# Kernel optimization log

Measured on AMD Instinct MI355X. Metric: run time of the kernel, lower is better.

Reference implementation:

```python
import jax, jax.numpy as jnp
import numpy as np

DEPTH, HEADS, DIM_HEAD = 3, 8, 64
DIM = 512
MAX_SEQ = 2048
INNER = HEADS * DIM_HEAD  # 512
FF_HID = 4 * DIM          # 2048
EPS = 1e-5


def sparsemax(z):
    # z: (..., n); sparsemax projection onto the simplex (Martins & Astudillo 2016)
    n = z.shape[-1]
    z_sorted = jnp.flip(jnp.sort(z, axis=-1), axis=-1)            # descending
    cs = jnp.cumsum(z_sorted, axis=-1)
    ks = jnp.arange(1, n + 1, dtype=z.dtype)
    support = 1.0 + ks * z_sorted > cs                            # bool
    k_z = jnp.sum(support, axis=-1, keepdims=True)                # int support size
    cs_k = jnp.take_along_axis(cs, k_z - 1, axis=-1)
    tau = (cs_k - 1.0) / k_z.astype(z.dtype)
    return jnp.maximum(z - tau, 0.0)


def layernorm(x, g, b):
    mu = jnp.mean(x, axis=-1, keepdims=True)
    var = jnp.mean(jnp.square(x - mu), axis=-1, keepdims=True)
    return (x - mu) * jax.lax.rsqrt(var + EPS) * g + b


def setup_inputs() -> dict:
    key = jax.random.key(0)
    ks = jax.random.split(key, 12)
    s = 0.02
    inp = {
        "x": jax.random.normal(ks[0], (8, 1024, DIM), dtype=jnp.float32),
        "proj_w": jax.random.normal(ks[1], (DIM, DIM), dtype=jnp.float32) * s,
        "proj_b": jnp.zeros((DIM,), dtype=jnp.float32),
        "pos_emb": jax.random.normal(ks[2], (MAX_SEQ, DIM), dtype=jnp.float32) * s,
        "ln1_g": jnp.ones((DEPTH, DIM), dtype=jnp.float32),
        "ln1_b": jnp.zeros((DEPTH, DIM), dtype=jnp.float32),
        "wqkv": jax.random.normal(ks[3], (DEPTH, DIM, 3 * INNER), dtype=jnp.float32) * s,
        "wout": jax.random.normal(ks[4], (DEPTH, INNER, DIM), dtype=jnp.float32) * s,
        "bout": jnp.zeros((DEPTH, DIM), dtype=jnp.float32),
        "ln2_g": jnp.ones((DEPTH, DIM), dtype=jnp.float32),
        "ln2_b": jnp.zeros((DEPTH, DIM), dtype=jnp.float32),
        "w1": jax.random.normal(ks[5], (DEPTH, DIM, 2 * FF_HID), dtype=jnp.float32) * s,
        "b1": jnp.zeros((DEPTH, 2 * FF_HID), dtype=jnp.float32),
        "w2": jax.random.normal(ks[6], (DEPTH, FF_HID, DIM), dtype=jnp.float32) * s,
        "b2": jnp.zeros((DEPTH, DIM), dtype=jnp.float32),
    }
    return inp


def reference(x, proj_w, proj_b, pos_emb, ln1_g, ln1_b, wqkv, wout, bout,
              ln2_g, ln2_b, w1, b1, w2, b2):
    B, S, D = x.shape
    scale = DIM_HEAD ** -0.5
    x = x @ proj_w + proj_b                       # projection
    x = x + pos_emb[:S][None, :, :]               # positional embedding
    for l in range(DEPTH):
        # --- attention block (Residual(PreNorm(Attention))) ---
        h = layernorm(x, ln1_g[l], ln1_b[l])
        qkv = h @ wqkv[l]                         # (B,S,3*INNER)
        q, k, v = jnp.split(qkv, 3, axis=-1)
        rs = lambda t: t.reshape(B, S, HEADS, DIM_HEAD).transpose(0, 2, 1, 3)
        q, k, v = rs(q), rs(k), rs(v)             # (B,H,S,Dh)
        sim = jnp.einsum('bhid,bhjd->bhij', q, k) * scale
        attn = sparsemax(sim)
        out = jnp.einsum('bhij,bhjd->bhid', attn, v)
        out = out.transpose(0, 2, 1, 3).reshape(B, S, INNER)
        x = x + (out @ wout[l] + bout[l])
        # --- feedforward block (Residual(PreNorm(GEGLU FFN))) ---
        h = layernorm(x, ln2_g[l], ln2_b[l])
        hh = h @ w1[l] + b1[l]                    # (B,S,2*FF_HID)
        a, g = jnp.split(hh, 2, axis=-1)
        ff = (a * jax.nn.gelu(g, approximate=False)) @ w2[l] + b2[l]
        x = x + ff
    return jnp.mean(x, axis=1)                    # (B, D) mean pool
```

## Files before the change

kernel.cpp:

```cpp
#include <hip/hip_runtime.h>
#include <stdint.h>

typedef unsigned short u16;
typedef __attribute__((ext_vector_type(8))) short short8;
typedef __attribute__((ext_vector_type(4))) float f32x4;

__device__ __forceinline__ float bf2f(u16 u){
  union { unsigned u; float f; } v; v.u = ((unsigned)u) << 16; return v.f;
}
__device__ __forceinline__ u16 f2bf(float f){
  union { float f; unsigned u; } v; v.f = f;
  unsigned u = v.u;
  return (u16)((u + 0x7FFFu + ((u >> 16) & 1u)) >> 16);
}
__device__ __forceinline__ void g2lds16(const u16* g, u16* lds){
  __builtin_amdgcn_global_load_lds(
      (const __attribute__((address_space(1))) unsigned int*)g,
      (__attribute__((address_space(3))) unsigned int*)lds, 16, 0, 0);
}
__device__ __forceinline__ float gelu_fast(float g){
  float u2 = g * (1.5957691216057308f + 0.0713548162726f * g * g);
  return g * __builtin_amdgcn_rcpf(1.0f + __expf(-u2));
}

__global__ void k_flag(const unsigned* __restrict__ ln1g, int* __restrict__ flag){
  if (threadIdx.x == 0 && blockIdx.x == 0)
    *flag = (ln1g[0] == 0x3F800000u) ? 0 : 1;
}

__global__ void k_cvt_f32(const void* __restrict__ src, float* __restrict__ dst, int n,
                          const int* __restrict__ flag){
  int i = blockIdx.x * blockDim.x + threadIdx.x;
  if (i < n) dst[i] = (*flag) ? bf2f(((const u16*)src)[i]) : ((const float*)src)[i];
}
__global__ void k_cvt_f32_v8(const void* __restrict__ src, float* __restrict__ dst,
                             const int* __restrict__ flag){
  int i = blockIdx.x * blockDim.x + threadIdx.x;
  if (*flag){
    short8 v = ((const short8*)src)[i];
    float o[8];
    #pragma unroll
    for (int j = 0; j < 8; ++j) o[j] = bf2f((u16)v[j]);
    ((float4*)dst)[i*2]   = *(const float4*)o;
    ((float4*)dst)[i*2+1] = *(const float4*)(o + 4);
  } else {
    ((float4*)dst)[i*2]   = ((const float4*)src)[i*2];
    ((float4*)dst)[i*2+1] = ((const float4*)src)[i*2+1];
  }
}
__global__ void k_cvt_bf16(const void* __restrict__ src, u16* __restrict__ dst, int n,
                           const int* __restrict__ flag){
  int i = blockIdx.x * blockDim.x + threadIdx.x;
  if (i < n) dst[i] = (*flag) ? ((const u16*)src)[i] : f2bf(((const float*)src)[i]);
}
__global__ void k_cvt_bf16_v8(const void* __restrict__ src, u16* __restrict__ dst,
                              const int* __restrict__ flag){
  int i = blockIdx.x * blockDim.x + threadIdx.x;
  if (*flag){
    ((uint4*)dst)[i] = ((const uint4*)src)[i];
  } else {
    float4 a = ((const float4*)src)[i*2];
    float4 b = ((const float4*)src)[i*2+1];
    u16 o[8] = { f2bf(a.x), f2bf(a.y), f2bf(a.z), f2bf(a.w),
                 f2bf(b.x), f2bf(b.y), f2bf(b.z), f2bf(b.w) };
    ((uint4*)dst)[i] = *(const uint4*)o;
  }
}

__global__ void k_transpose(const void* __restrict__ src, u16* __restrict__ dst,
                            int K, int N, const int* __restrict__ flag){
  __shared__ u16 tile[32][33];
  int n0 = blockIdx.x * 32, k0 = blockIdx.y * 32;
  size_t zsrc = (size_t)blockIdx.z * K * N;
  size_t zdst = (size_t)blockIdx.z * N * K;
  int tx = threadIdx.x & 31, ty = threadIdx.x >> 5;
  bool isbf = (*flag) != 0;
  const float* sf = (const float*)src; const u16* sb = (const u16*)src;
  #pragma unroll
  for (int p = 0; p < 4; ++p){
    int kk = k0 + p*8 + ty, nn = n0 + tx;
    size_t idx = zsrc + (size_t)kk * N + nn;
    tile[tx][p*8+ty] = isbf ? sb[idx] : f2bf(sf[idx]);
  }
  __syncthreads();
  #pragma unroll
  for (int p = 0; p < 4; ++p){
    int nn = n0 + p*8 + ty, kk = k0 + tx;
    dst[zdst + (size_t)nn * K + kk] = tile[p*8+ty][tx];
  }
}

__global__ __launch_bounds__(256) void k_ln(const float* __restrict__ x,
                                            const float* __restrict__ g,
                                            const float* __restrict__ b,
                                            u16* __restrict__ out){
  int wv = threadIdx.x >> 6, lane = threadIdx.x & 63;
  int row = blockIdx.x * 4 + wv;
  const float* xr = x + (size_t)row * 512 + lane * 8;
  float4 v0 = *(const float4*)xr;
  float4 v1 = *(const float4*)(xr + 4);
  float s  = v0.x+v0.y+v0.z+v0.w + v1.x+v1.y+v1.z+v1.w;
  float ss = v0.x*v0.x+v0.y*v0.y+v0.z*v0.z+v0.w*v0.w
           + v1.x*v1.x+v1.y*v1.y+v1.z*v1.z+v1.w*v1.w;
  #pragma unroll
  for (int off = 1; off < 64; off <<= 1){ s += __shfl_xor(s, off, 64); ss += __shfl_xor(ss, off, 64); }
  float mu = s * (1.f/512.f);
  float var = ss * (1.f/512.f) - mu*mu;
  float rs = rsqrtf(var + 1e-5f);
  const float* gp = g + lane*8; const float* bp = b + lane*8;
  float4 g0 = *(const float4*)gp, g1 = *(const float4*)(gp+4);
  float4 b0 = *(const float4*)bp, b1 = *(const float4*)(bp+4);
  u16 o[8];
  o[0]=f2bf((v0.x-mu)*rs*g0.x+b0.x); o[1]=f2bf((v0.y-mu)*rs*g0.y+b0.y);
  o[2]=f2bf((v0.z-mu)*rs*g0.z+b0.z); o[3]=f2bf((v0.w-mu)*rs*g0.w+b0.w);
  o[4]=f2bf((v1.x-mu)*rs*g1.x+b1.x); o[5]=f2bf((v1.y-mu)*rs*g1.y+b1.y);
  o[6]=f2bf((v1.z-mu)*rs*g1.z+b1.z); o[7]=f2bf((v1.w-mu)*rs*g1.w+b1.w);
  *(uint4*)(out + (size_t)row*512 + lane*8) = *(const uint4*)o;
}

__global__ __launch_bounds__(256) void k_gemm(const u16* __restrict__ A,
                                              const u16* __restrict__ Wt, int K, int mode,
                                              float* __restrict__ xres, u16* __restrict__ out16,
                                              const float* __restrict__ bias,
                                              const float* __restrict__ pos){
  __shared__ u16 As[128*64];
  __shared__ u16 Bs[128*64];
  const int tid = threadIdx.x;
  const int wv = tid >> 6, lane = tid & 63;
  const int lm = lane & 15, lq = lane >> 4;
  const int wm = (wv >> 1) * 64, wn = (wv & 1) * 64;
  const int m0 = blockIdx.y * 128, n0 = blockIdx.x * 128;
  const int lrow = lane >> 3;
  const int scol = ((lane & 7) ^ lrow) << 3;
  f32x4 acc[4][4];
  #pragma unroll
  for (int i = 0; i < 4; ++i)
    #pragma unroll
    for (int j = 0; j < 4; ++j){ f32x4 z = {0.f,0.f,0.f,0.f}; acc[i][j] = z; }

  for (int k0 = 0; k0 < K; k0 += 64){
    #pragma unroll
    for (int it = 0; it < 4; ++it){
      int ci = wv*4 + it;
      int row = ci*8 + lrow;
      g2lds16(&A [(size_t)(m0 + row) * K + k0 + scol], &As[ci*512]);
      g2lds16(&Wt[(size_t)(n0 + row) * K + k0 + scol], &Bs[ci*512]);
    }
    __syncthreads();
    #pragma unroll
    for (int kk = 0; kk < 2; ++kk){
      short8 af[4], bf[4];
      #pragma unroll
      for (int t = 0; t < 4; ++t){
        int cs = ((kk*4 + lq) ^ (lm & 7)) << 3;
        af[t] = *(const short8*)&As[(wm + t*16 + lm)*64 + cs];
        bf[t] = *(const short8*)&Bs[(wn + t*16 + lm)*64 + cs];
      }
      #pragma unroll
      for (int i = 0; i < 4; ++i)
        #pragma unroll
        for (int j = 0; j < 4; ++j)
          acc[i][j] = __builtin_amdgcn_mfma_f32_16x16x32_bf16(af[i], bf[j], acc[i][j], 0, 0, 0);
    }
    __syncthreads();
  }
  #pragma unroll
  for (int i = 0; i < 4; ++i)
    #pragma unroll
    for (int j = 0; j < 4; ++j)
      #pragma unroll
      for (int r = 0; r < 4; ++r){
        int row = m0 + wm + i*16 + lq*4 + r;
        int col = n0 + wn + j*16 + lm;
        float v = acc[i][j][r];
        if (mode == 0){
          xres[(size_t)row*512 + col] = v + bias[col] + pos[(size_t)(row & 1023)*512 + col];
        } else if (mode == 1){
          int part = col >> 9, within = col & 511;
          int head = within >> 6, dh = within & 63;
          int b = row >> 10, s = row & 1023;
          int bh = b*8 + head;
          size_t o;
          if (part < 2) o = (size_t)part*4194304 + (((size_t)bh*1024 + s) << 6) + dh;
          else          o = (size_t)8388608 + (size_t)bh*65536 + (size_t)dh*1024 + s;
          out16[o] = f2bf(v);
        } else {
          size_t idx = (size_t)row*512 + col;
          xres[idx] = xres[idx] + v + bias[col];
        }
      }
}

__global__ __launch_bounds__(256) void k_gemm64(const u16* __restrict__ A,
                                                const u16* __restrict__ Wt, int K, int mode,
                                                float* __restrict__ xres,
                                                const float* __restrict__ bias,
                                                const float* __restrict__ pos){
  __shared__ u16 As[64*64];
  __shared__ u16 Bs[128*64];
  const int tid = threadIdx.x;
  const int wv = tid >> 6, lane = tid & 63;
  const int lm = lane & 15, lq = lane >> 4;
  const int wm = (wv >> 1) * 32, wn = (wv & 1) * 64;
  const int m0 = blockIdx.y * 64, n0 = blockIdx.x * 128;
  const int lrow = lane >> 3;
  const int scol = ((lane & 7) ^ lrow) << 3;
  f32x4 acc[2][4];
  #pragma unroll
  for (int i = 0; i < 2; ++i)
    #pragma unroll
    for (int j = 0; j < 4; ++j){ f32x4 z = {0.f,0.f,0.f,0.f}; acc[i][j] = z; }

  for (int k0 = 0; k0 < K; k0 += 64){
    #pragma unroll
    for (int it = 0; it < 2; ++it){
      int ci = wv*2 + it;
      int row = ci*8 + lrow;
      g2lds16(&A[(size_t)(m0 + row) * K + k0 + scol], &As[ci*512]);
    }
    #pragma unroll
    for (int it = 0; it < 4; ++it){
      int ci = wv*4 + it;
      int row = ci*8 + lrow;
      g2lds16(&Wt[(size_t)(n0 + row) * K + k0 + scol], &Bs[ci*512]);
    }
    __syncthreads();
    #pragma unroll
    for (int kk = 0; kk < 2; ++kk){
      short8 af[2], bf[4];
      int cs = ((kk*4 + lq) ^ (lm & 7)) << 3;
      #pragma unroll
      for (int t = 0; t < 2; ++t)
        af[t] = *(const short8*)&As[(wm + t*16 + lm)*64 + cs];
      #pragma unroll
      for (int t = 0; t < 4; ++t)
        bf[t] = *(const short8*)&Bs[(wn + t*16 + lm)*64 + cs];
      #pragma unroll
      for (int i = 0; i < 2; ++i)
        #pragma unroll
        for (int j = 0; j < 4; ++j)
          acc[i][j] = __builtin_amdgcn_mfma_f32_16x16x32_bf16(af[i], bf[j], acc[i][j], 0, 0, 0);
    }
    __syncthreads();
  }
  #pragma unroll
  for (int i = 0; i < 2; ++i)
    #pragma unroll
    for (int j = 0; j < 4; ++j)
      #pragma unroll
      for (int r = 0; r < 4; ++r){
        int row = m0 + wm + i*16 + lq*4 + r;
        int col = n0 + wn + j*16 + lm;
        float v = acc[i][j][r];
        if (mode == 0){
          xres[(size_t)row*512 + col] = v + bias[col] + pos[(size_t)(row & 1023)*512 + col];
        } else {
          size_t idx = (size_t)row*512 + col;
          xres[idx] = xres[idx] + v + bias[col];
        }
      }
}

__global__ __launch_bounds__(256) void k_ff1_geglu64(const u16* __restrict__ A,
                                                     const u16* __restrict__ W1t,
                                                     const float* __restrict__ b1,
                                                     u16* __restrict__ ffh){
  __shared__ u16 As[64*64];
  __shared__ u16 Ba[128*64];
  __shared__ u16 Bg[128*64];
  const int tid = threadIdx.x;
  const int wv = tid >> 6, lane = tid & 63;
  const int lm = lane & 15, lq = lane >> 4;
  const int wm = (wv >> 1) * 32, wn = (wv & 1) * 64;
  const int m0 = blockIdx.y * 64, n0 = blockIdx.x * 128;
  const int lrow = lane >> 3;
  const int scol = ((lane & 7) ^ lrow) << 3;
  const int K = 512;
  f32x4 aa[2][4], ag[2][4];
  #pragma unroll
  for (int i = 0; i < 2; ++i)
    #pragma unroll
    for (int j = 0; j < 4; ++j){ f32x4 z = {0.f,0.f,0.f,0.f}; aa[i][j] = z; ag[i][j] = z; }
  for (int k0 = 0; k0 < K; k0 += 64){
    #pragma unroll
    for (int it = 0; it < 2; ++it){
      int ci = wv*2 + it;
      int row = ci*8 + lrow;
      g2lds16(&A[(size_t)(m0 + row) * K + k0 + scol], &As[ci*512]);
    }
    #pragma unroll
    for (int it = 0; it < 4; ++it){
      int ci = wv*4 + it;
      int row = ci*8 + lrow;
      g2lds16(&W1t[(size_t)(n0 + row) * K + k0 + scol],        &Ba[ci*512]);
      g2lds16(&W1t[(size_t)(2048 + n0 + row) * K + k0 + scol], &Bg[ci*512]);
    }
    __syncthreads();
    #pragma unroll
    for (int kk = 0; kk < 2; ++kk){
      short8 af[2], ba[4], bg[4];
      int cs = ((kk*4 + lq) ^ (lm & 7)) << 3;
      #pragma unroll
      for (int t = 0; t < 2; ++t)
        af[t] = *(const short8*)&As[(wm + t*16 + lm)*64 + cs];
      #pragma unroll
      for (int t = 0; t < 4; ++t){
        ba[t] = *(const short8*)&Ba[(wn + t*16 + lm)*64 + cs];
        bg[t] = *(const short8*)&Bg[(wn + t*16 + lm)*64 + cs];
      }
      #pragma unroll
      for (int i = 0; i < 2; ++i)
        #pragma unroll
        for (int j = 0; j < 4; ++j){
          aa[i][j] = __builtin_amdgcn_mfma_f32_16x16x32_bf16(af[i], ba[j], aa[i][j], 0, 0, 0);
          ag[i][j] = __builtin_amdgcn_mfma_f32_16x16x32_bf16(af[i], bg[j], ag[i][j], 0, 0, 0);
        }
    }
    __syncthreads();
  }
  #pragma unroll
  for (int i = 0; i < 2; ++i)
    #pragma unroll
    for (int j = 0; j < 4; ++j)
      #pragma unroll
      for (int r = 0; r < 4; ++r){
        int row = m0 + wm + i*16 + lq*4 + r;
        int n = n0 + wn + j*16 + lm;
        float a = aa[i][j][r] + b1[n];
        float g = ag[i][j][r] + b1[2048 + n];
        ffh[(size_t)row*2048 + n] = f2bf(a * gelu_fast(g));
      }
}

__global__ __launch_bounds__(256) void k_attn2(const u16* __restrict__ qb,
                                               const u16* __restrict__ kb,
                                               const u16* __restrict__ vt,
                                               u16* __restrict__ aout){
  __shared__ u16 Sm[16*1024];
  const int tid = threadIdx.x;
  const int wv = tid >> 6, lane = tid & 63;
  const int lm = lane & 15, lq = lane >> 4;
  int fid = blockIdx.x;
  int nf = (fid & 7) * 512 + (fid >> 3);
  const int bh = nf >> 6;
  const int q0 = (nf & 63) * 16;
  const size_t base = (size_t)bh * 65536;
  const u16* qp = &qb[base + (size_t)(q0 + lm)*64 + lq*8];
  short8 qf0 = *(const short8*)qp;
  short8 qf1 = *(const short8*)(qp + 32);
  for (int kt = 0; kt < 16; ++kt){
    const u16* kp = &kb[base + (size_t)(kt*64 + wv*16 + lm)*64 + lq*8];
    short8 kf0 = *(const short8*)kp;
    short8 kf1 = *(const short8*)(kp + 32);
    f32x4 a = {0.f,0.f,0.f,0.f};
    a = __builtin_amdgcn_mfma_f32_16x16x32_bf16(qf0, kf0, a, 0, 0, 0);
    a = __builtin_amdgcn_mfma_f32_16x16x32_bf16(qf1, kf1, a, 0, 0, 0);
    int col = kt*64 + wv*16 + lm;
    int cc = col >> 3, c7 = col & 7;
    #pragma unroll
    for (int r = 0; r < 4; ++r){
      int row = lq*4 + r;
      Sm[row*1024 + ((cc ^ (row & 7)) << 3) + c7] = f2bf(a[r] * 0.125f);
    }
  }
  __syncthreads();
  #pragma unroll 1
  for (int rr = 0; rr < 4; ++rr){
    int row = wv*4 + rr;
    int r7 = row & 7;
    u16* lo = &Sm[row*1024 + ((lane ^ r7) << 3)];
    u16* hi = &Sm[row*1024 + (((64 + lane) ^ r7) << 3)];
    u16 zb[16];
    *(uint4*)zb       = *(const uint4*)lo;
    *(uint4*)(zb + 8) = *(const uint4*)hi;
    float z[16];
    #pragma unroll
    for (int i = 0; i < 16; ++i) z[i] = bf2f(zb[i]);
    float s0 = 0.f;
    #pragma unroll
    for (int i = 0; i < 16; ++i) s0 += z[i];
    #pragma unroll
    for (int off = 1; off < 64; off <<= 1) s0 += __shfl_xor(s0, off, 64);
    float tau = (s0 - 1.0f) * (1.0f/1024.0f);
    int prevc = 1024;
    #pragma unroll 1
    for (int it = 0; it < 32; ++it){
      float sz = 0.f; int c = 0;
      #pragma unroll
      for (int i = 0; i < 16; ++i){
        bool aq = z[i] > tau;
        sz += aq ? z[i] : 0.f;
        c  += (int)__popcll(__ballot(aq));
      }
      if (c >= prevc) break;
      #pragma unroll
      for (int off = 1; off < 64; off <<= 1) sz += __shfl_xor(sz, off, 64);
      tau = (sz - 1.0f) / (float)c;
      prevc = c;
    }
    u16 pb[16];
    #pragma unroll
    for (int i = 0; i < 16; ++i){
      float p = z[i] - tau;
      pb[i] = f2bf(p > 0.f ? p : 0.f);
    }
    *(uint4*)lo = *(const uint4*)pb;
    *(uint4*)hi = *(const uint4*)(pb + 8);
  }
  __syncthreads();
  f32x4 acc = {0.f,0.f,0.f,0.f};
  const u16* vrow = &vt[base + (size_t)(wv*16 + lm)*1024 + lq*8];
  for (int k0 = 0; k0 < 1024; k0 += 32){
    int cc = (k0 >> 3) + lq;
    short8 pa = *(const short8*)&Sm[lm*1024 + ((cc ^ (lm & 7)) << 3)];
    short8 vb = *(const short8*)(vrow + k0);
    acc = __builtin_amdgcn_mfma_f32_16x16x32_bf16(pa, vb, acc, 0, 0, 0);
  }
  int b = bh >> 3, h = bh & 7;
  #pragma unroll
  for (int r = 0; r < 4; ++r){
    int s = q0 + lq*4 + r;
    aout[((size_t)(b*1024 + s))*512 + h*64 + wv*16 + lm] = f2bf(acc[r]);
  }
}

__global__ __launch_bounds__(256) void k_pool1(const float* __restrict__ xres,
                                               float* __restrict__ part){
  int b = blockIdx.y, ch = blockIdx.x, tid = threadIdx.x;
  float a0 = 0.f, a1 = 0.f;
  for (int i = 0; i < 64; ++i){
    const float* r = xres + ((size_t)(b*1024 + ch*64 + i)) * 512;
    a0 += r[tid]; a1 += r[tid + 256];
  }
  part[((size_t)(b*16 + ch))*512 + tid]       = a0;
  part[((size_t)(b*16 + ch))*512 + tid + 256] = a1;
}
__global__ __launch_bounds__(512) void k_pool2(const float* __restrict__ part,
                                               void* __restrict__ out,
                                               const int* __restrict__ flag){
  int b = blockIdx.x, d = threadIdx.x;
  float s = 0.f;
  for (int c = 0; c < 16; ++c) s += part[((size_t)(b*16 + c))*512 + d];
  s *= (1.0f/1024.0f);
  if (*flag) ((u16*)out)[b*512 + d] = f2bf(s);
  else       ((float*)out)[b*512 + d] = s;
}

extern "C" void kernel_launch(void* const* d_in, const int* in_sizes, int n_in,
                              void* d_out, int out_size, void* d_ws, size_t ws_size,
                              hipStream_t stream){
  (void)in_sizes; (void)n_in; (void)out_size; (void)ws_size;
  char* w = (char*)d_ws;
  size_t off = 0;
  auto alloc = [&](size_t bytes) -> char* {
    char* p = w + off;
    off += (bytes + 255) & ~(size_t)255;
    return p;
  };
  int*   flag  = (int*)  alloc(4);
  float* xres  = (float*)alloc((size_t)8192*512*4);
  u16*   hb    = (u16*)  alloc((size_t)8192*512*2);
  u16*   qb    = (u16*)  alloc((size_t)8388608);
  u16*   kb    = (u16*)  alloc((size_t)8388608);
  u16*   vtb   = (u16*)  alloc((size_t)8388608);
  u16*   aoutb = (u16*)  alloc((size_t)8388608);
  u16*   ffh   = qb;
  u16*   pwT   = (u16*)  alloc((size_t)512*512*2);
  u16*   wqkvT = (u16*)  alloc((size_t)3*1536*512*2);
  u16*   woutT = (u16*)  alloc((size_t)3*512*512*2);
  u16*   w1T   = (u16*)  alloc((size_t)3*4096*512*2);
  u16*   w2T   = (u16*)  alloc((size_t)3*512*2048*2);
  float* posf  = (float*)alloc((size_t)1024*512*4);
  float* pbf   = (float*)alloc(512*4);
  float* ln1gf = (float*)alloc(1536*4);
  float* ln1bf = (float*)alloc(1536*4);
  float* ln2gf = (float*)alloc(1536*4);
  float* ln2bf = (float*)alloc(1536*4);
  float* boutf = (float*)alloc(1536*4);
  float* b1f   = (float*)alloc(12288*4);
  float* b2f   = (float*)alloc(1536*4);
  float* part  = (float*)alloc((size_t)8*16*512*4);

  const void* x_raw = d_in[0];  const void* projw = d_in[1];  const void* projb = d_in[2];
  const void* pose  = d_in[3];  const void* ln1g  = d_in[4];  const void* ln1b  = d_in[5];
  const void* wqkv  = d_in[6];  const void* wout  = d_in[7];  const void* bout  = d_in[8];
  const void* ln2g  = d_in[9];  const void* ln2b  = d_in[10]; const void* w1    = d_in[11];
  const void* b1    = d_in[12]; const void* w2    = d_in[13]; const void* b2    = d_in[14];

  k_flag<<<1, 1, 0, stream>>>((const unsigned*)ln1g, flag);

  k_transpose<<<dim3(16, 16, 1), 256, 0, stream>>>(projw, pwT,   512,  512, flag);
  k_transpose<<<dim3(48, 16, 3), 256, 0, stream>>>(wqkv,  wqkvT, 512, 1536, flag);
  k_transpose<<<dim3(16, 16, 3), 256, 0, stream>>>(wout,  woutT, 512,  512, flag);
  k_transpose<<<dim3(128,16, 3), 256, 0, stream>>>(w1,    w1T,   512, 4096, flag);
  k_transpose<<<dim3(16, 64, 3), 256, 0, stream>>>(w2,    w2T,  2048,  512, flag);

  k_cvt_f32<<<2,    256, 0, stream>>>(projb, pbf,    512,    flag);
  k_cvt_f32_v8<<<256, 256, 0, stream>>>(pose, posf, flag);
  k_cvt_f32<<<6,    256, 0, stream>>>(ln1g,  ln1gf,  1536,   flag);
  k_cvt_f32<<<6,    256, 0, stream>>>(ln1b,  ln1bf,  1536,   flag);
  k_cvt_f32<<<6,    256, 0, stream>>>(ln2g,  ln2gf,  1536,   flag);
  k_cvt_f32<<<6,    256, 0, stream>>>(ln2b,  ln2bf,  1536,   flag);
  k_cvt_f32<<<6,    256, 0, stream>>>(bout,  boutf,  1536,   flag);
  k_cvt_f32<<<48,   256, 0, stream>>>(b1,    b1f,    12288,  flag);
  k_cvt_f32<<<6,    256, 0, stream>>>(b2,    b2f,    1536,   flag);
  k_cvt_bf16_v8<<<2048, 256, 0, stream>>>(x_raw, hb, flag);

  k_gemm64<<<dim3(4, 128), 256, 0, stream>>>(hb, pwT, 512, 0, xres, pbf, posf);

  for (int l = 0; l < 3; ++l){
    k_ln<<<2048, 256, 0, stream>>>(xres, ln1gf + l*512, ln1bf + l*512, hb);
    k_gemm<<<dim3(12, 64), 256, 0, stream>>>(hb, wqkvT + (size_t)l*1536*512, 512, 1,
                                             nullptr, qb, nullptr, nullptr);
    k_attn2<<<dim3(4096), 256, 0, stream>>>(qb, kb, vtb, aoutb);
    k_gemm64<<<dim3(4, 128), 256, 0, stream>>>(aoutb, woutT + (size_t)l*512*512, 512, 2,
                                               xres, boutf + l*512, nullptr);
    k_ln<<<2048, 256, 0, stream>>>(xres, ln2gf + l*512, ln2bf + l*512, hb);
    k_ff1_geglu64<<<dim3(16, 128), 256, 0, stream>>>(hb, w1T + (size_t)l*4096*512,
                                                     b1f + l*4096, ffh);
    k_gemm64<<<dim3(4, 128), 256, 0, stream>>>(ffh, w2T + (size_t)l*512*2048, 2048, 2,
                                               xres, b2f + l*512, nullptr);
  }
  k_pool1<<<dim3(16, 8), 256, 0, stream>>>(xres, part);
  k_pool2<<<8, 512, 0, stream>>>(part, d_out, flag);
}
```

Before: 1.065 ms.

## Widen attention block to 16 waves with split-K PV and LDS reduction

The sparsemax attention kernel now launches with 1024 threads instead of 256. Each of the 16 waves computes one 64-column key tile of QK^T, handles one row of the sparsemax threshold iteration, and computes a quarter of the PV product per output slice. The four partial PV results are reduced through a new shared-memory buffer before the bf16 store. The idea is to cut each wave's serial loops and raise parallelism per block, at the cost of more LDS, an extra barrier, and possibly lower occupancy. The sparsemax loop also now reduces and uses a fast reciprocal before its convergence check.

```diff
diff --git a/kernel.cpp b/kernel.cpp
--- a/kernel.cpp
+++ b/kernel.cpp
@@ -332,11 +332,12 @@
       }
 }
 
-__global__ __launch_bounds__(256) void k_attn2(const u16* __restrict__ qb,
-                                               const u16* __restrict__ kb,
-                                               const u16* __restrict__ vt,
-                                               u16* __restrict__ aout){
+__global__ __launch_bounds__(1024) void k_attn2(const u16* __restrict__ qb,
+                                                const u16* __restrict__ kb,
+                                                const u16* __restrict__ vt,
+                                                u16* __restrict__ aout){
   __shared__ u16 Sm[16*1024];
+  __shared__ float Pp[4*16*64];
   const int tid = threadIdx.x;
   const int wv = tid >> 6, lane = tid & 63;
   const int lm = lane & 15, lq = lane >> 4;
@@ -348,26 +349,28 @@
   const u16* qp = &qb[base + (size_t)(q0 + lm)*64 + lq*8];
   short8 qf0 = *(const short8*)qp;
   short8 qf1 = *(const short8*)(qp + 32);
-  for (int kt = 0; kt < 16; ++kt){
-    const u16* kp = &kb[base + (size_t)(kt*64 + wv*16 + lm)*64 + lq*8];
-    short8 kf0 = *(const short8*)kp;
-    short8 kf1 = *(const short8*)(kp + 32);
-    f32x4 a = {0.f,0.f,0.f,0.f};
-    a = __builtin_amdgcn_mfma_f32_16x16x32_bf16(qf0, kf0, a, 0, 0, 0);
-    a = __builtin_amdgcn_mfma_f32_16x16x32_bf16(qf1, kf1, a, 0, 0, 0);
-    int col = kt*64 + wv*16 + lm;
-    int cc = col >> 3, c7 = col & 7;
-    #pragma unroll
-    for (int r = 0; r < 4; ++r){
-      int row = lq*4 + r;
-      Sm[row*1024 + ((cc ^ (row & 7)) << 3) + c7] = f2bf(a[r] * 0.125f);
+  {
+    const int kt = wv;
+    #pragma unroll
+    for (int j = 0; j < 4; ++j){
+      const u16* kp = &kb[base + (size_t)(kt*64 + j*16 + lm)*64 + lq*8];
+      short8 kf0 = *(const short8*)kp;
+      short8 kf1 = *(const short8*)(kp + 32);
+      f32x4 a = {0.f,0.f,0.f,0.f};
+      a = __builtin_amdgcn_mfma_f32_16x16x32_bf16(qf0, kf0, a, 0, 0, 0);
+      a = __builtin_amdgcn_mfma_f32_16x16x32_bf16(qf1, kf1, a, 0, 0, 0);
+      int col = kt*64 + j*16 + lm;
+      int cc = col >> 3, c7 = col & 7;
+      #pragma unroll
+      for (int r = 0; r < 4; ++r){
+        int row = lq*4 + r;
+        Sm[row*1024 + ((cc ^ (row & 7)) << 3) + c7] = f2bf(a[r] * 0.125f);
+      }
     }
   }
   __syncthreads();
-  #pragma unroll 1
-  for (int rr = 0; rr < 4; ++rr){
-    int row = wv*4 + rr;
-    int r7 = row & 7;
+  {
+    const int row = wv, r7 = row & 7;
     u16* lo = &Sm[row*1024 + ((lane ^ r7) << 3)];
     u16* hi = &Sm[row*1024 + (((64 + lane) ^ r7) << 3)];
     u16 zb[16];
@@ -392,10 +395,10 @@
         sz += aq ? z[i] : 0.f;
         c  += (int)__popcll(__ballot(aq));
       }
+      #pragma unroll
+      for (int off = 1; off < 64; off <<= 1) sz += __shfl_xor(sz, off, 64);
+      tau = (sz - 1.0f) * __builtin_amdgcn_rcpf((float)c);
       if (c >= prevc) break;
-      #pragma unroll
-      for (int off = 1; off < 64; off <<= 1) sz += __shfl_xor(sz, off, 64);
-      tau = (sz - 1.0f) / (float)c;
       prevc = c;
     }
     u16 pb[16];
@@ -405,22 +408,31 @@
       pb[i] = f2bf(p > 0.f ? p : 0.f);
     }
     *(uint4*)lo = *(const uint4*)pb;
-    *(uint4*)hi = *(const uint4*)(pb + 8);
+    *(uint4*)(hi) = *(const uint4*)(pb + 8);
   }
   __syncthreads();
-  f32x4 acc = {0.f,0.f,0.f,0.f};
-  const u16* vrow = &vt[base + (size_t)(wv*16 + lm)*1024 + lq*8];
-  for (int k0 = 0; k0 < 1024; k0 += 32){
-    int cc = (k0 >> 3) + lq;
-    short8 pa = *(const short8*)&Sm[lm*1024 + ((cc ^ (lm & 7)) << 3)];
-    short8 vb = *(const short8*)(vrow + k0);
-    acc = __builtin_amdgcn_mfma_f32_16x16x32_bf16(pa, vb, acc, 0, 0, 0);
-  }
-  int b = bh >> 3, h = bh & 7;
-  #pragma unroll
-  for (int r = 0; r < 4; ++r){
-    int s = q0 + lq*4 + r;
-    aout[((size_t)(b*1024 + s))*512 + h*64 + wv*16 + lm] = f2bf(acc[r]);
+  {
+    const int ds = wv & 3, kc = wv >> 2;
+    f32x4 acc = {0.f,0.f,0.f,0.f};
+    const u16* vrow = &vt[base + (size_t)(ds*16 + lm)*1024 + lq*8];
+    #pragma unroll
+    for (int k0 = kc*256; k0 < kc*256 + 256; k0 += 32){
+      int cc = (k0 >> 3) + lq;
+      short8 pa = *(const short8*)&Sm[lm*1024 + ((cc ^ (lm & 7)) << 3)];
+      short8 vb = *(const short8*)(vrow + k0);
+      acc = __builtin_amdgcn_mfma_f32_16x16x32_bf16(pa, vb, acc, 0, 0, 0);
+    }
+    #pragma unroll
+    for (int r = 0; r < 4; ++r)
+      Pp[(kc*16 + lq*4 + r)*64 + ds*16 + lm] = acc[r];
+  }
+  __syncthreads();
+  {
+    int s = tid >> 6, d = tid & 63;
+    int o = s*64 + d;
+    float v = Pp[o] + Pp[1024 + o] + Pp[2048 + o] + Pp[3072 + o];
+    int b = bh >> 3, h = bh & 7;
+    aout[((size_t)(b*1024 + q0 + s))*512 + h*64 + d] = f2bf(v);
   }
 }
 
@@ -512,7 +524,7 @@
     k_ln<<<2048, 256, 0, stream>>>(xres, ln1gf + l*512, ln1bf + l*512, hb);
     k_gemm<<<dim3(12, 64), 256, 0, stream>>>(hb, wqkvT + (size_t)l*1536*512, 512, 1,
                                              nullptr, qb, nullptr, nullptr);
-    k_attn2<<<dim3(4096), 256, 0, stream>>>(qb, kb, vtb, aoutb);
+    k_attn2<<<dim3(4096), 1024, 0, stream>>>(qb, kb, vtb, aoutb);
     k_gemm64<<<dim3(4, 128), 256, 0, stream>>>(aoutb, woutT + (size_t)l*512*512, 512, 2,
                                                xres, boutf + l*512, nullptr);
     k_ln<<<2048, 256, 0, stream>>>(xres, ln2gf + l*512, ln2bf + l*512, hb);
```

Measured after the change: 1.100 ms. 1.03x slower.

## Warm-start sparsemax threshold from row statistics and process two rows at once

Applied to the files above, without the earlier changes.

The sparsemax threshold search now starts from an estimate built from the row's mean, standard deviation and max (a Gaussian-tail heuristic) instead of tau=(sum-1)/n. It then iterates a Newton-style update from above or below, capped at 48 iterations. Two rows are processed together per wave so the shuffle reductions and ballots interleave and expose more instruction-level parallelism. The aim is fewer sequential threshold iterations per row. The cost is extra register pressure, and the heuristic start may take more iterations on some inputs or converge to a slightly different tau. An unused conversion kernel is also deleted.

```diff
diff --git a/kernel.cpp b/kernel.cpp
--- a/kernel.cpp
+++ b/kernel.cpp
@@ -47,11 +47,6 @@
     ((float4*)dst)[i*2]   = ((const float4*)src)[i*2];
     ((float4*)dst)[i*2+1] = ((const float4*)src)[i*2+1];
   }
-}
-__global__ void k_cvt_bf16(const void* __restrict__ src, u16* __restrict__ dst, int n,
-                           const int* __restrict__ flag){
-  int i = blockIdx.x * blockDim.x + threadIdx.x;
-  if (i < n) dst[i] = (*flag) ? ((const u16*)src)[i] : f2bf(((const float*)src)[i]);
 }
 __global__ void k_cvt_bf16_v8(const void* __restrict__ src, u16* __restrict__ dst,
                               const int* __restrict__ flag){
@@ -365,47 +360,89 @@
   }
   __syncthreads();
   #pragma unroll 1
-  for (int rr = 0; rr < 4; ++rr){
-    int row = wv*4 + rr;
-    int r7 = row & 7;
-    u16* lo = &Sm[row*1024 + ((lane ^ r7) << 3)];
-    u16* hi = &Sm[row*1024 + (((64 + lane) ^ r7) << 3)];
-    u16 zb[16];
-    *(uint4*)zb       = *(const uint4*)lo;
-    *(uint4*)(zb + 8) = *(const uint4*)hi;
-    float z[16];
-    #pragma unroll
-    for (int i = 0; i < 16; ++i) z[i] = bf2f(zb[i]);
-    float s0 = 0.f;
-    #pragma unroll
-    for (int i = 0; i < 16; ++i) s0 += z[i];
-    #pragma unroll
-    for (int off = 1; off < 64; off <<= 1) s0 += __shfl_xor(s0, off, 64);
-    float tau = (s0 - 1.0f) * (1.0f/1024.0f);
-    int prevc = 1024;
+  for (int pp = 0; pp < 2; ++pp){
+    int rowA = wv*4 + pp*2, rowB = rowA + 1;
+    int aA7 = rowA & 7, aB7 = rowB & 7;
+    u16* loA = &Sm[rowA*1024 + ((lane ^ aA7) << 3)];
+    u16* hiA = &Sm[rowA*1024 + (((64 + lane) ^ aA7) << 3)];
+    u16* loB = &Sm[rowB*1024 + ((lane ^ aB7) << 3)];
+    u16* hiB = &Sm[rowB*1024 + (((64 + lane) ^ aB7) << 3)];
+    u16 zbA[16], zbB[16];
+    *(uint4*)zbA       = *(const uint4*)loA;
+    *(uint4*)(zbA + 8) = *(const uint4*)hiA;
+    *(uint4*)zbB       = *(const uint4*)loB;
+    *(uint4*)(zbB + 8) = *(const uint4*)hiB;
+    float zA[16], zB[16];
+    #pragma unroll
+    for (int i = 0; i < 16; ++i){ zA[i] = bf2f(zbA[i]); zB[i] = bf2f(zbB[i]); }
+    float sA = 0.f, ssA = 0.f, mxA = zA[0];
+    float sB = 0.f, ssB = 0.f, mxB = zB[0];
+    #pragma unroll
+    for (int i = 0; i < 16; ++i){
+      sA += zA[i]; ssA = fmaf(zA[i], zA[i], ssA); mxA = fmaxf(mxA, zA[i]);
+      sB += zB[i]; ssB = fmaf(zB[i], zB[i], ssB); mxB = fmaxf(mxB, zB[i]);
+    }
+    #pragma unroll
+    for (int off = 1; off < 64; off <<= 1){
+      sA  += __shfl_xor(sA,  off, 64);  sB  += __shfl_xor(sB,  off, 64);
+      ssA += __shfl_xor(ssA, off, 64);  ssB += __shfl_xor(ssB, off, 64);
+      mxA  = fmaxf(mxA, __shfl_xor(mxA, off, 64));
+      mxB  = fmaxf(mxB, __shfl_xor(mxB, off, 64));
+    }
+    float muA = sA * (1.0f/1024.0f), muB = sB * (1.0f/1024.0f);
+    float vA = fmaxf(ssA * (1.0f/1024.0f) - muA*muA, 1e-12f);
+    float vB = fmaxf(ssB * (1.0f/1024.0f) - muB*muB, 1e-12f);
+    float sgA = sqrtf(vA), sgB = sqrtf(vB);
+    float wA = 0.69314718f * (10.0f + __log2f(sgA));
+    float wB = 0.69314718f * (10.0f + __log2f(sgB));
+    float argA = fmaxf(1.63f * wA - 0.5257f, 0.0f);
+    float argB = fmaxf(1.63f * wB - 0.5257f, 0.0f);
+    float uA = fminf(fmaxf((sqrtf(argA) - 1.0625f) * (1.0f/0.815f), 0.0f), 3.5f);
+    float uB = fminf(fmaxf((sqrtf(argB) - 1.0625f) * (1.0f/0.815f), 0.0f), 3.5f);
+    float tauA = fminf(fmaf(sgA, uA, muA), mxA - 0.0009765625f);
+    float tauB = fminf(fmaf(sgB, uB, muB), mxB - 0.0009765625f);
+    int prevcA = 1025, prevcB = 1025;
+    bool actA = true, actB = true;
     #pragma unroll 1
-    for (int it = 0; it < 32; ++it){
-      float sz = 0.f; int c = 0;
+    for (int it = 0; it < 48; ++it){
+      float s2A = 0.f, s2B = 0.f; int cA = 0, cB = 0;
       #pragma unroll
       for (int i = 0; i < 16; ++i){
-        bool aq = z[i] > tau;
-        sz += aq ? z[i] : 0.f;
-        c  += (int)__popcll(__ballot(aq));
-      }
-      if (c >= prevc) break;
-      #pragma unroll
-      for (int off = 1; off < 64; off <<= 1) sz += __shfl_xor(sz, off, 64);
-      tau = (sz - 1.0f) / (float)c;
-      prevc = c;
-    }
-    u16 pb[16];
+        float pA = zA[i] - tauA;
+        float pB = zB[i] - tauB;
+        s2A += (pA > 0.f ? pA : 0.f);
+        s2B += (pB > 0.f ? pB : 0.f);
+        cA += (int)__popcll(__ballot(zA[i] > tauA));
+        cB += (int)__popcll(__ballot(zB[i] > tauB));
+      }
+      #pragma unroll
+      for (int off = 1; off < 64; off <<= 1){
+        s2A += __shfl_xor(s2A, off, 64);
+        s2B += __shfl_xor(s2B, off, 64);
+      }
+      if (actA){
+        tauA += (s2A - 1.0f) / (float)cA;
+        actA = (cA != prevcA);
+        prevcA = cA;
+      }
+      if (actB){
+        tauB += (s2B - 1.0f) / (float)cB;
+        actB = (cB != prevcB);
+        prevcB = cB;
+      }
+      if (!actA && !actB) break;
+    }
+    u16 tA[16], tB[16];
     #pragma unroll
     for (int i = 0; i < 16; ++i){
-      float p = z[i] - tau;
-      pb[i] = f2bf(p > 0.f ? p : 0.f);
-    }
-    *(uint4*)lo = *(const uint4*)pb;
-    *(uint4*)hi = *(const uint4*)(pb + 8);
+      float pA = zA[i] - tauA; pA = pA > 0.f ? pA : 0.f;
+      float pB = zB[i] - tauB; pB = pB > 0.f ? pB : 0.f;
+      tA[i] = f2bf(pA); tB[i] = f2bf(pB);
+    }
+    *(uint4*)loA = *(const uint4*)tA;
+    *(uint4*)hiA = *(const uint4*)(tA + 8);
+    *(uint4*)loB = *(const uint4*)tB;
+    *(uint4*)hiB = *(const uint4*)(tB + 8);
   }
   __syncthreads();
   f32x4 acc = {0.f,0.f,0.f,0.f};
```

Result: no change. 1.053 ms (-1.1%).
